# Kernel optimization log

Measured on AMD Instinct MI355X. Metric: run time of the kernel, lower is better.

The kernel has to match this reference:

```python
import jax, jax.numpy as jnp
import numpy as np

EMBED_DIM = 512  # channels C
B, H, W = 2, 64, 64


def _conv1x1(x, w, b):
    # x: [B, C, H, W]; w: [C_out, C_in]; b: [C_out]  (1x1 conv == per-pixel linear)
    return jnp.einsum('bchw,dc->bdhw', x, w) + b[None, :, None, None]


def setup_inputs() -> dict:
    key = jax.random.key(0)
    ks = jax.random.split(key, 9)
    C = EMBED_DIM
    s = 1.0 / np.sqrt(C)
    x = jax.random.normal(ks[0], (B, C, H, W), dtype=jnp.float32)
    wq = jax.random.normal(ks[1], (C, C), dtype=jnp.float32) * s
    bq = jax.random.normal(ks[2], (C,), dtype=jnp.float32) * 0.01
    wk = jax.random.normal(ks[3], (C, C), dtype=jnp.float32) * s
    bk = jax.random.normal(ks[4], (C,), dtype=jnp.float32) * 0.01
    wv = jax.random.normal(ks[5], (C, C), dtype=jnp.float32) * s
    bv = jax.random.normal(ks[6], (C,), dtype=jnp.float32) * 0.01
    wo = jax.random.normal(ks[7], (C, C), dtype=jnp.float32) * s
    bo = jax.random.normal(ks[8], (C,), dtype=jnp.float32) * 0.01
    return {"x": x, "wq": wq, "bq": bq, "wk": wk, "bk": bk,
            "wv": wv, "bv": bv, "wo": wo, "bo": bo}


def reference(x, wq, bq, wk, bk, wv, bv, wo, bo):
    b, c, h, w = x.shape
    n = h * w
    q = _conv1x1(x, wq, bq).reshape(b, c, n)
    k = _conv1x1(x, wk, bk).reshape(b, c, n)
    v = _conv1x1(x, wv, bv).reshape(b, c, n)
    # scores = q^T @ k over channel dim -> [b, n, n]; scale by sqrt(C) (scale=True)
    scores = jnp.einsum('bcn,bcm->bnm', q, k) / jnp.sqrt(jnp.asarray(c, x.dtype))
    attn = jax.nn.softmax(scores, axis=-1)
    # output = v @ attn^T -> [b, c, n]
    out = jnp.einsum('bcm,bnm->bcn', v, attn).reshape(b, c, h, w)
    return _conv1x1(out, wo, bo)
```

## Files before the change

### kernel.cpp

```cpp
#include <hip/hip_runtime.h>
#include <stdint.h>

typedef short s16x8 __attribute__((ext_vector_type(8)));
typedef unsigned short u16x8 __attribute__((ext_vector_type(8)));
typedef float f32x4 __attribute__((ext_vector_type(4)));

__device__ __forceinline__ float bf2f(unsigned short u) {
  union { unsigned u; float f; } c; c.u = ((unsigned)u) << 16; return c.f;
}
__device__ __forceinline__ unsigned short f2bf(float f) {
  union { float f; unsigned u; } c; c.f = f;
  unsigned u = c.u + 0x7fffu + ((c.u >> 16) & 1u);
  return (unsigned short)(u >> 16);
}

__device__ __forceinline__ void g2l16(const void* g, void* l) {
  __builtin_amdgcn_global_load_lds(
      (const __attribute__((address_space(1))) void*)(unsigned long long)g,
      (__attribute__((address_space(3))) void*)(unsigned)(unsigned long long)l,
      16, 0, 0);
}

template <int MODE, typename OutT>
__global__ __launch_bounds__(256) void gemm_abt(
    const unsigned short* __restrict__ A, int lda,
    const unsigned short* __restrict__ Bt, int ldb,
    OutT* __restrict__ C, int ldc,
    const float* __restrict__ bias,
    float* __restrict__ rowsum,
    int M, int N, int K, int nsplit,
    long long sA, long long sBt, long long sC, long long sSplit,
    float scale)
{
  __shared__ __align__(16) unsigned short smem[128 * 136];
  unsigned short* As = smem;
  unsigned short* Bs = smem + 128 * 64;

  const int ks = blockIdx.z % nsplit;
  const int bz = blockIdx.z / nsplit;
  A  += (long long)bz * sA;
  Bt += (long long)bz * sBt;
  C  += (long long)bz * sC + (long long)ks * sSplit;

  const int tile_m = blockIdx.y * 128;
  const int tile_n = blockIdx.x * 128;

  const int tid  = threadIdx.x;
  const int wid  = tid >> 6;
  const int lane = tid & 63;
  const int wm = (wid >> 1) * 64;
  const int wn = (wid & 1) * 64;
  const int lr = lane & 15;
  const int lq = lane >> 4;

  const int srow = lane >> 3;
  const int scol = ((lane & 7) ^ (srow & 7)) * 8;

  f32x4 acc[4][4];
  const f32x4 zero4 = {0.f, 0.f, 0.f, 0.f};
  #pragma unroll
  for (int i = 0; i < 4; ++i)
    #pragma unroll
    for (int j = 0; j < 4; ++j) acc[i][j] = zero4;

  const unsigned short* Arow = A  + (long long)tile_m * lda;
  const unsigned short* Brow = Bt + (long long)tile_n * ldb;

  const int kLen = K / nsplit;
  const int kBeg = ks * kLen;

  for (int k0 = kBeg; k0 < kBeg + kLen; k0 += 64) {
    #pragma unroll
    for (int c = 0; c < 4; ++c) {
      const int chunk = wid * 4 + c;
      const int row = chunk * 8 + srow;
      g2l16(Arow + (long long)row * lda + k0 + scol, As + chunk * 512);
      g2l16(Brow + (long long)row * ldb + k0 + scol, Bs + chunk * 512);
    }
    __syncthreads();
    #pragma unroll
    for (int kss = 0; kss < 2; ++kss) {
      const int cch = kss * 4 + lq;
      s16x8 af[4], bfr[4];
      #pragma unroll
      for (int i = 0; i < 4; ++i) {
        const int row = wm + i * 16 + lr;
        af[i] = *(const s16x8*)&As[row * 64 + ((cch ^ (row & 7)) * 8)];
      }
      #pragma unroll
      for (int j = 0; j < 4; ++j) {
        const int row = wn + j * 16 + lr;
        bfr[j] = *(const s16x8*)&Bs[row * 64 + ((cch ^ (row & 7)) * 8)];
      }
      #pragma unroll
      for (int i = 0; i < 4; ++i)
        #pragma unroll
        for (int j = 0; j < 4; ++j)
          acc[i][j] = __builtin_amdgcn_mfma_f32_16x16x32_bf16(af[i], bfr[j], acc[i][j], 0, 0, 0);
    }
    __syncthreads();
  }

  if constexpr (MODE == 0) {
    #pragma unroll
    for (int i = 0; i < 4; ++i) {
      const int row0 = tile_m + wm + i * 16 + lq * 4;
      #pragma unroll
      for (int j = 0; j < 4; ++j) {
        const int col = tile_n + wn + j * 16 + lr;
        #pragma unroll
        for (int r = 0; r < 4; ++r) {
          float v = acc[i][j][r] * scale;
          if (bias) v += bias[row0 + r];
          C[(long long)(row0 + r) * ldc + col] = (OutT)v;
        }
      }
    }
  } else {
    #pragma unroll
    for (int i = 0; i < 4; ++i) {
      const int lrow0 = wm + i * 16 + lq * 4;
      float rsum[4] = {0.f, 0.f, 0.f, 0.f};
      #pragma unroll
      for (int j = 0; j < 4; ++j) {
        const int lcol = wn + j * 16 + lr;
        float bcol = 0.f;
        if (MODE == 1 && bias) bcol = bias[tile_n + lcol];
        #pragma unroll
        for (int r = 0; r < 4; ++r) {
          float v = acc[i][j][r] * scale + bcol;
          if (MODE == 2) { v = __expf(v); rsum[r] += v; }
          smem[(lrow0 + r) * 136 + lcol] = f2bf(v);
        }
      }
      if (MODE == 2) {
        #pragma unroll
        for (int r = 0; r < 4; ++r) {
          float s = rsum[r];
          s += __shfl_xor(s, 1); s += __shfl_xor(s, 2);
          s += __shfl_xor(s, 4); s += __shfl_xor(s, 8);
          if (lr == 0)
            atomicAdd(&rowsum[(long long)bz * M + tile_m + lrow0 + r], s);
        }
      }
    }
    __syncthreads();
    const int row = tid >> 1;
    const int cb = (tid & 1) * 64;
    unsigned short* Cg = (unsigned short*)C;
    #pragma unroll
    for (int k = 0; k < 8; ++k) {
      u16x8 v = *(const u16x8*)&smem[row * 136 + cb + k * 8];
      *(u16x8*)&Cg[(long long)(tile_m + row) * ldc + tile_n + cb + k * 8] = v;
    }
  }
}

__global__ __launch_bounds__(256) void cvt_weights(
    const float* __restrict__ wq, const float* __restrict__ wk,
    const float* __restrict__ wv, const float* __restrict__ wo,
    const float* __restrict__ bq, const float* __restrict__ bk,
    const float* __restrict__ bv,
    unsigned short* __restrict__ wb, float* __restrict__ bqkv,
    float* __restrict__ rowsum, int n)
{
  const int i = blockIdx.x * 256 + threadIdx.x;
  if (i < n) {
    wb[i]         = f2bf(wq[i]);
    wb[n + i]     = f2bf(wk[i]);
    wb[2 * n + i] = f2bf(wv[i]);
    wb[3 * n + i] = f2bf(wo[i]);
  }
  if (i < 512) {
    bqkv[i]        = bq[i];
    bqkv[512 + i]  = bk[i];
    bqkv[1024 + i] = bv[i];
  }
  if (i < 8192) rowsum[i] = 0.f;
}

__global__ __launch_bounds__(256) void transpose_cn(
    const float* __restrict__ x, unsigned short* __restrict__ xT,
    int C, int N)
{
  __shared__ float tile[32][33];
  const long long boff = (long long)blockIdx.z * C * N;
  const int n0 = blockIdx.x * 32;
  const int c0 = blockIdx.y * 32;
  const int tx = threadIdx.x;
  const int ty = threadIdx.y;
  #pragma unroll
  for (int k = 0; k < 32; k += 8)
    tile[ty + k][tx] = x[boff + (long long)(c0 + ty + k) * N + n0 + tx];
  __syncthreads();
  #pragma unroll
  for (int k = 0; k < 32; k += 8)
    xT[boff + (long long)(n0 + ty + k) * C + c0 + tx] = f2bf(tile[tx][ty + k]);
}

__global__ __launch_bounds__(256) void transpose_bf(
    const unsigned short* __restrict__ src, int srcLd, long long sSrc,
    unsigned short* __restrict__ dst, int dstLd, long long sDst,
    int R, int Cc)
{
  __shared__ unsigned short tile[32][33];
  const int r0 = blockIdx.x * 32;
  const int c0 = blockIdx.y * 32;
  const int tx = threadIdx.x;
  const int ty = threadIdx.y;
  const long long so = (long long)blockIdx.z * sSrc;
  const long long dofs = (long long)blockIdx.z * sDst;
  #pragma unroll
  for (int k = 0; k < 32; k += 8)
    tile[ty + k][tx] = src[so + (long long)(r0 + ty + k) * srcLd + c0 + tx];
  __syncthreads();
  #pragma unroll
  for (int k = 0; k < 32; k += 8)
    dst[dofs + (long long)(c0 + ty + k) * dstLd + r0 + tx] = tile[tx][ty + k];
}

__global__ __launch_bounds__(256) void reduce4_norm(
    const unsigned short* __restrict__ p, long long L,
    const float* __restrict__ rowsum, unsigned short* __restrict__ o)
{
  const long long i = 8LL * (blockIdx.x * 256 + threadIdx.x);
  const int b = (int)(i >> 21);
  const int n = (int)((i >> 9) & 4095);
  const float inv = 1.0f / rowsum[b * 4096 + n];
  u16x8 a = *(const u16x8*)&p[i];
  u16x8 bb = *(const u16x8*)&p[L + i];
  u16x8 c = *(const u16x8*)&p[2 * L + i];
  u16x8 d = *(const u16x8*)&p[3 * L + i];
  u16x8 w;
  #pragma unroll
  for (int j = 0; j < 8; ++j)
    w[j] = f2bf(((bf2f(a[j]) + bf2f(bb[j])) + (bf2f(c[j]) + bf2f(d[j]))) * inv);
  *(u16x8*)&o[i] = w;
}

extern "C" void kernel_launch(void* const* d_in, const int* in_sizes, int n_in,
                              void* d_out, int out_size, void* d_ws, size_t ws_size,
                              hipStream_t stream) {
  (void)in_sizes; (void)n_in; (void)out_size; (void)ws_size;
  const float* x  = (const float*)d_in[0];
  const float* wq = (const float*)d_in[1];
  const float* bq = (const float*)d_in[2];
  const float* wk = (const float*)d_in[3];
  const float* bk = (const float*)d_in[4];
  const float* wv = (const float*)d_in[5];
  const float* bv = (const float*)d_in[6];
  const float* wo = (const float*)d_in[7];
  const float* bo = (const float*)d_in[8];
  float* out = (float*)d_out;

  const int Cc = 512, N = 4096, Bn = 2, C3 = 1536;
  const int CC = Cc * Cc;
  const long long NC  = (long long)N * Cc;
  const long long NC3 = (long long)N * C3;
  const long long NN  = (long long)N * N;

  char* wsb = (char*)d_ws;
  unsigned short* wb   = (unsigned short*)wsb;
  float*          bqkv = (float*)(wsb + 4LL * CC * 2);
  unsigned short* xT   = (unsigned short*)(wsb + 4LL * CC * 2 + 8192);
  unsigned short* qkvT = xT + Bn * NC;
  unsigned short* vv   = qkvT + Bn * NC3;
  unsigned short* aO   = vv + Bn * NC;
  unsigned short* S    = aO + Bn * NC;
  unsigned short* part = S + Bn * NN;
  float*          rsum = (float*)(part + 4LL * Bn * NC);

  unsigned short* wob = wb + 3LL * CC;
  const float inv_sqrt_c = 0.044194173824159216f;

  cvt_weights<<<dim3((CC + 255) / 256), 256, 0, stream>>>(
      wq, wk, wv, wo, bq, bk, bv, wb, bqkv, rsum, CC);
  transpose_cn<<<dim3(N / 32, Cc / 32, Bn), dim3(32, 8), 0, stream>>>(x, xT, Cc, N);

  gemm_abt<1, unsigned short><<<dim3(C3 / 128, N / 128, Bn), 256, 0, stream>>>(
      xT, Cc, wb, Cc, qkvT, C3, bqkv, nullptr, N, C3, Cc, 1,
      NC, 0, NC3, 0, 1.0f);
  transpose_bf<<<dim3(N / 32, Cc / 32, Bn), dim3(32, 8), 0, stream>>>(
      qkvT + 1024, C3, NC3, vv, N, NC, N, Cc);
  gemm_abt<2, unsigned short><<<dim3(N / 128, N / 128, Bn), 256, 0, stream>>>(
      qkvT, C3, qkvT + 512, C3, S, N, nullptr, rsum, N, N, Cc, 1,
      NC3, NC3, NN, 0, inv_sqrt_c);
  gemm_abt<1, unsigned short><<<dim3(Cc / 128, N / 128, Bn * 4), 256, 0, stream>>>(
      S, N, vv, N, part, Cc, nullptr, nullptr, N, Cc, N, 4,
      NN, NC, NC, (long long)Bn * NC, 1.0f);
  reduce4_norm<<<dim3((int)((Bn * NC) / 2048)), 256, 0, stream>>>(
      part, (long long)Bn * NC, rsum, aO);
  gemm_abt<0, float><<<dim3(N / 128, Cc / 128, Bn), 256, 0, stream>>>(
      wob, Cc, aO, Cc, out, N, bo, nullptr, Cc, N, Cc, 1,
      0, NC, NC, 0, 1.0f);
}
```

Before: 282.9 us.

## Fold output projection into value weights and fuse normalization with atomic split-K

Precomputes Wp = Wo·Wv and a combined bias Wo·bv+bo, so V is produced already projected and the separate output-projection GEMM disappears. The PV GEMM now writes fp32 output directly: it normalizes by the row sums in its epilogue and accumulates two K-splits with atomicAdd. This removes the transpose, reduce and final GEMM kernels. The cost is a memset and fp32 atomics on the output, plus a change in rounding because the weight product is stored in bf16.

```diff
diff --git a/kernel.cpp b/kernel.cpp
--- a/kernel.cpp
+++ b/kernel.cpp
@@ -101,18 +101,19 @@
     __syncthreads();
   }
 
-  if constexpr (MODE == 0) {
+  if constexpr (MODE == 3) {
     #pragma unroll
     for (int i = 0; i < 4; ++i) {
       const int row0 = tile_m + wm + i * 16 + lq * 4;
       #pragma unroll
       for (int j = 0; j < 4; ++j) {
         const int col = tile_n + wn + j * 16 + lr;
+        const float inv = 1.0f / rowsum[(long long)bz * N + col];
         #pragma unroll
         for (int r = 0; r < 4; ++r) {
-          float v = acc[i][j][r] * scale;
-          if (bias) v += bias[row0 + r];
-          C[(long long)(row0 + r) * ldc + col] = (OutT)v;
+          float v = acc[i][j][r] * inv;
+          if (ks == 0) v += bias[row0 + r];
+          atomicAdd((float*)&C[(long long)(row0 + r) * ldc + col], v);
         }
       }
     }
@@ -160,23 +161,37 @@
     const float* __restrict__ wq, const float* __restrict__ wk,
     const float* __restrict__ wv, const float* __restrict__ wo,
     const float* __restrict__ bq, const float* __restrict__ bk,
-    const float* __restrict__ bv,
-    unsigned short* __restrict__ wb, float* __restrict__ bqkv,
+    unsigned short* __restrict__ wqk_b, unsigned short* __restrict__ wvT_b,
+    unsigned short* __restrict__ wo_b, float* __restrict__ bqk,
     float* __restrict__ rowsum, int n)
 {
   const int i = blockIdx.x * 256 + threadIdx.x;
   if (i < n) {
-    wb[i]         = f2bf(wq[i]);
-    wb[n + i]     = f2bf(wk[i]);
-    wb[2 * n + i] = f2bf(wv[i]);
-    wb[3 * n + i] = f2bf(wo[i]);
+    wqk_b[i]     = f2bf(wq[i]);
+    wqk_b[n + i] = f2bf(wk[i]);
+    wvT_b[i]     = f2bf(wv[(i & 511) * 512 + (i >> 9)]);
+    wo_b[i]      = f2bf(wo[i]);
   }
   if (i < 512) {
-    bqkv[i]        = bq[i];
-    bqkv[512 + i]  = bk[i];
-    bqkv[1024 + i] = bv[i];
+    bqk[i]       = bq[i];
+    bqk[512 + i] = bk[i];
   }
   if (i < 8192) rowsum[i] = 0.f;
+}
+
+__global__ __launch_bounds__(256) void bias_pp(
+    const float* __restrict__ wo, const float* __restrict__ bv,
+    const float* __restrict__ bo, float* __restrict__ bpp)
+{
+  const int w = threadIdx.x >> 6, lane = threadIdx.x & 63;
+  const int d = blockIdx.x * 4 + w;
+  const float* row = wo + (long long)d * 512;
+  float s = 0.f;
+  #pragma unroll
+  for (int c = 0; c < 512; c += 64) s += row[c + lane] * bv[c + lane];
+  #pragma unroll
+  for (int o = 32; o > 0; o >>= 1) s += __shfl_xor(s, o, 64);
+  if (lane == 0) bpp[d] = s + bo[d];
 }
 
 __global__ __launch_bounds__(256) void transpose_cn(
@@ -198,50 +213,10 @@
     xT[boff + (long long)(n0 + ty + k) * C + c0 + tx] = f2bf(tile[tx][ty + k]);
 }
 
-__global__ __launch_bounds__(256) void transpose_bf(
-    const unsigned short* __restrict__ src, int srcLd, long long sSrc,
-    unsigned short* __restrict__ dst, int dstLd, long long sDst,
-    int R, int Cc)
-{
-  __shared__ unsigned short tile[32][33];
-  const int r0 = blockIdx.x * 32;
-  const int c0 = blockIdx.y * 32;
-  const int tx = threadIdx.x;
-  const int ty = threadIdx.y;
-  const long long so = (long long)blockIdx.z * sSrc;
-  const long long dofs = (long long)blockIdx.z * sDst;
-  #pragma unroll
-  for (int k = 0; k < 32; k += 8)
-    tile[ty + k][tx] = src[so + (long long)(r0 + ty + k) * srcLd + c0 + tx];
-  __syncthreads();
-  #pragma unroll
-  for (int k = 0; k < 32; k += 8)
-    dst[dofs + (long long)(c0 + ty + k) * dstLd + r0 + tx] = tile[tx][ty + k];
-}
-
-__global__ __launch_bounds__(256) void reduce4_norm(
-    const unsigned short* __restrict__ p, long long L,
-    const float* __restrict__ rowsum, unsigned short* __restrict__ o)
-{
-  const long long i = 8LL * (blockIdx.x * 256 + threadIdx.x);
-  const int b = (int)(i >> 21);
-  const int n = (int)((i >> 9) & 4095);
-  const float inv = 1.0f / rowsum[b * 4096 + n];
-  u16x8 a = *(const u16x8*)&p[i];
-  u16x8 bb = *(const u16x8*)&p[L + i];
-  u16x8 c = *(const u16x8*)&p[2 * L + i];
-  u16x8 d = *(const u16x8*)&p[3 * L + i];
-  u16x8 w;
-  #pragma unroll
-  for (int j = 0; j < 8; ++j)
-    w[j] = f2bf(((bf2f(a[j]) + bf2f(bb[j])) + (bf2f(c[j]) + bf2f(d[j]))) * inv);
-  *(u16x8*)&o[i] = w;
-}
-
 extern "C" void kernel_launch(void* const* d_in, const int* in_sizes, int n_in,
                               void* d_out, int out_size, void* d_ws, size_t ws_size,
                               hipStream_t stream) {
-  (void)in_sizes; (void)n_in; (void)out_size; (void)ws_size;
+  (void)in_sizes; (void)n_in; (void)ws_size;
   const float* x  = (const float*)d_in[0];
   const float* wq = (const float*)d_in[1];
   const float* bq = (const float*)d_in[2];
@@ -253,44 +228,46 @@
   const float* bo = (const float*)d_in[8];
   float* out = (float*)d_out;
 
-  const int Cc = 512, N = 4096, Bn = 2, C3 = 1536;
+  const int Cc = 512, N = 4096, Bn = 2;
   const int CC = Cc * Cc;
   const long long NC  = (long long)N * Cc;
-  const long long NC3 = (long long)N * C3;
+  const long long NC2 = (long long)N * 1024;
   const long long NN  = (long long)N * N;
 
   char* wsb = (char*)d_ws;
-  unsigned short* wb   = (unsigned short*)wsb;
-  float*          bqkv = (float*)(wsb + 4LL * CC * 2);
-  unsigned short* xT   = (unsigned short*)(wsb + 4LL * CC * 2 + 8192);
-  unsigned short* qkvT = xT + Bn * NC;
-  unsigned short* vv   = qkvT + Bn * NC3;
-  unsigned short* aO   = vv + Bn * NC;
-  unsigned short* S    = aO + Bn * NC;
-  unsigned short* part = S + Bn * NN;
-  float*          rsum = (float*)(part + 4LL * Bn * NC);
-
-  unsigned short* wob = wb + 3LL * CC;
+  unsigned short* wqk_b = (unsigned short*)wsb;
+  unsigned short* wvT_b = wqk_b + 2LL * CC;
+  unsigned short* wo_b  = wvT_b + CC;
+  unsigned short* Wp    = wo_b + CC;
+  float*          bqk   = (float*)(Wp + CC);
+  float*          bpp   = bqk + 1024;
+  float*          rsum  = bpp + 512;
+  unsigned short* xT    = (unsigned short*)(rsum + 8192);
+  unsigned short* qkT   = xT + Bn * NC;
+  unsigned short* vo    = qkT + Bn * NC2;
+  unsigned short* S     = vo + Bn * NC;
+
   const float inv_sqrt_c = 0.044194173824159216f;
 
   cvt_weights<<<dim3((CC + 255) / 256), 256, 0, stream>>>(
-      wq, wk, wv, wo, bq, bk, bv, wb, bqkv, rsum, CC);
+      wq, wk, wv, wo, bq, bk, wqk_b, wvT_b, wo_b, bqk, rsum, CC);
+  bias_pp<<<dim3(128), 256, 0, stream>>>(wo, bv, bo, bpp);
+  gemm_abt<1, unsigned short><<<dim3(4, 4, 1), 256, 0, stream>>>(
+      wo_b, 512, wvT_b, 512, Wp, 512, nullptr, nullptr,
+      512, 512, 512, 1, 0, 0, 0, 0, 1.0f);
   transpose_cn<<<dim3(N / 32, Cc / 32, Bn), dim3(32, 8), 0, stream>>>(x, xT, Cc, N);
 
-  gemm_abt<1, unsigned short><<<dim3(C3 / 128, N / 128, Bn), 256, 0, stream>>>(
-      xT, Cc, wb, Cc, qkvT, C3, bqkv, nullptr, N, C3, Cc, 1,
-      NC, 0, NC3, 0, 1.0f);
-  transpose_bf<<<dim3(N / 32, Cc / 32, Bn), dim3(32, 8), 0, stream>>>(
-      qkvT + 1024, C3, NC3, vv, N, NC, N, Cc);
+  gemm_abt<1, unsigned short><<<dim3(8, N / 128, Bn), 256, 0, stream>>>(
+      xT, Cc, wqk_b, Cc, qkT, 1024, bqk, nullptr, N, 1024, Cc, 1,
+      NC, 0, NC2, 0, 1.0f);
   gemm_abt<2, unsigned short><<<dim3(N / 128, N / 128, Bn), 256, 0, stream>>>(
-      qkvT, C3, qkvT + 512, C3, S, N, nullptr, rsum, N, N, Cc, 1,
-      NC3, NC3, NN, 0, inv_sqrt_c);
-  gemm_abt<1, unsigned short><<<dim3(Cc / 128, N / 128, Bn * 4), 256, 0, stream>>>(
-      S, N, vv, N, part, Cc, nullptr, nullptr, N, Cc, N, 4,
-      NN, NC, NC, (long long)Bn * NC, 1.0f);
-  reduce4_norm<<<dim3((int)((Bn * NC) / 2048)), 256, 0, stream>>>(
-      part, (long long)Bn * NC, rsum, aO);
-  gemm_abt<0, float><<<dim3(N / 128, Cc / 128, Bn), 256, 0, stream>>>(
-      wob, Cc, aO, Cc, out, N, bo, nullptr, Cc, N, Cc, 1,
+      qkT, 1024, qkT + 512, 1024, S, N, nullptr, rsum, N, N, Cc, 1,
+      NC2, NC2, NN, 0, inv_sqrt_c);
+  gemm_abt<1, unsigned short><<<dim3(N / 128, 4, Bn), 256, 0, stream>>>(
+      Wp, 512, xT, 512, vo, N, nullptr, nullptr, 512, N, Cc, 1,
       0, NC, NC, 0, 1.0f);
-}
+  hipMemsetAsync(out, 0, (size_t)out_size * sizeof(float), stream);
+  gemm_abt<3, float><<<dim3(N / 128, 4, Bn * 2), 256, 0, stream>>>(
+      vo, N, S, N, out, N, bpp, rsum, 512, N, N, 2,
+      NC, NN, NC, 0, 1.0f);
+}
```

Result: no change. 285.2 us (+0.8%).
